# Kernel optimization log

Hardware: AMD Instinct MI355X
Metric: run time of the kernel (lower is better)

## Reference

```python
import jax, jax.numpy as jnp
import numpy as np

K = 5                      # spline kernel_size per dim
NEG = -1e30                # finite -inf stand-in for max-scatter init
_COMBO = np.indices((2, 2, 2)).reshape(3, 8).T   # [8,3] corner offsets of the deg-1 B-spline support
_STRIDE = np.array([1, K, K * K])


def spline_basis(pseudo):
    # pseudo: [E,3] in [0,1]; open degree-1 B-spline, kernel_size K per dim.
    v = jnp.clip(pseudo, 0.0, 1.0) * (K - 1)
    i0 = jnp.clip(jnp.floor(v), 0, K - 2)
    f = v - i0                                   # [E,3] fractional part
    c = jnp.asarray(_COMBO)                      # [8,3]
    w = jnp.prod(jnp.where(c[None] == 1, f[:, None, :], 1.0 - f[:, None, :]), axis=2)  # [E,8]
    k = jnp.sum((i0.astype(jnp.int32)[:, None, :] + c[None]) * jnp.asarray(_STRIDE)[None, None, :], axis=2)  # [E,8]
    return w, k


def spline_conv(x, src, dst, pseudo, W, root, bias):
    # x:[N,Fin], W:[K^3,Fin,Fout]. Gather-spline-scatter, mean aggregation + root weight + bias.
    N = x.shape[0]
    U = jnp.einsum('ni,kio->nko', x, W)          # [N,K^3,Fout] all-kernel transform (dense GEMM)
    bw, kidx = spline_basis(pseudo)              # [E,8], [E,8]
    msg = jnp.sum(bw[:, :, None] * U[src[:, None], kidx], axis=1)  # [E,Fout]
    deg = jnp.zeros((N,), x.dtype).at[dst].add(1.0)
    agg = jnp.zeros((N, W.shape[2]), x.dtype).at[dst].add(msg) / jnp.maximum(deg, 1.0)[:, None]
    return agg + x @ root + bias


def weighted_max_pool(x, w, cluster, C):
    # keep features of the max-attention-weight node in each voxel cluster
    seg_w = jnp.full((C,), NEG, x.dtype).at[cluster].max(w)
    winner = w >= seg_w[cluster]
    pooled = jnp.full((C, x.shape[1]), NEG, x.dtype).at[cluster].max(jnp.where(winner[:, None], x, NEG))
    return jnp.where(pooled <= NEG / 2, 0.0, pooled)


def dense_max_pool(x, cluster, C):
    pooled = jnp.full((C, x.shape[1]), NEG, x.dtype).at[cluster].max(x)
    return jnp.where(pooled <= NEG / 2, 0.0, pooled)


def setup_inputs() -> dict:
    key = jax.random.key(0)
    ks = iter(jax.random.split(key, 80))
    N = [30000, 10000, 4000, 1500, 600]
    E = [360000, 120000, 48000, 18000, 7200]
    Fin = [1, 32, 64, 64, 64]
    Fout = [32, 64, 64, 64, 64]
    Cs = [10000, 4000, 1500, 600, 128]
    d = {"x": jax.random.normal(next(ks), (N[0], 1), jnp.float32)}
    for l in range(5):
        d[f"src{l}"] = jax.random.randint(next(ks), (E[l],), 0, N[l], jnp.int32)
        d[f"dst{l}"] = jax.random.randint(next(ks), (E[l],), 0, N[l], jnp.int32)
        d[f"pseudo{l}"] = jax.random.uniform(next(ks), (E[l], 3), jnp.float32)
    for l in range(5):
        d[f"cluster{l+1}"] = jax.random.randint(next(ks), (N[l],), 0, Cs[l], jnp.int32)
    for l in range(5):
        d[f"W{l+1}"] = 0.1 * jax.random.normal(next(ks), (K ** 3, Fin[l], Fout[l]), jnp.float32)
        d[f"root{l+1}"] = 0.1 * jax.random.normal(next(ks), (Fin[l], Fout[l]), jnp.float32)
        d[f"b{l+1}"] = jnp.zeros((Fout[l],), jnp.float32)
    for l, fdim in enumerate([32, 64, 64, 64]):
        d[f"attw{l+1}"] = 0.1 * jax.random.normal(next(ks), (fdim, 2), jnp.float32)
        d[f"attb{l+1}"] = jnp.zeros((2,), jnp.float32)
    d["fcw"] = 0.05 * jax.random.normal(next(ks), (512, 10), jnp.float32)
    d["fcb"] = jnp.zeros((10,), jnp.float32)
    return d


def reference(x, src0, dst0, pseudo0, src1, dst1, pseudo1, src2, dst2, pseudo2,
              src3, dst3, pseudo3, src4, dst4, pseudo4,
              cluster1, cluster2, cluster3, cluster4, cluster5,
              W1, root1, b1, W2, root2, b2, W3, root3, b3, W4, root4, b4, W5, root5, b5,
              attw1, attb1, attw2, attb2, attw3, attb3, attw4, attb4, fcw, fcb):
    h = jax.nn.elu(spline_conv(x, src0, dst0, pseudo0, W1, root1, b1))
    h = weighted_max_pool(h, (h @ attw1 + attb1)[:, 0], cluster1, 10000)
    h = jax.nn.elu(spline_conv(h, src1, dst1, pseudo1, W2, root2, b2))
    h = weighted_max_pool(h, (h @ attw2 + attb2)[:, 0], cluster2, 4000)
    h = jax.nn.elu(spline_conv(h, src2, dst2, pseudo2, W3, root3, b3))
    h = weighted_max_pool(h, (h @ attw3 + attb3)[:, 0], cluster3, 1500)
    h = jax.nn.elu(spline_conv(h, src3, dst3, pseudo3, W4, root4, b4))
    h = weighted_max_pool(h, (h @ attw4 + attb4)[:, 0], cluster4, 600)
    h = jax.nn.relu(spline_conv(h, src4, dst4, pseudo4, W5, root5, b5))
    h = dense_max_pool(h, cluster5, 128)        # [128, 64] = 16 graphs x 8 voxels
    z = h.reshape(-1, 512)                      # [16, 8*64]
    return jax.nn.log_softmax(z @ fcw + fcb, axis=1)
```

## Files before the change

### kernel.cpp

```cpp
#include <hip/hip_runtime.h>
#include <math.h>

#define KS 5

typedef __bf16 bf16x8 __attribute__((ext_vector_type(8)));
typedef float f32x4 __attribute__((ext_vector_type(4)));
typedef unsigned long long u64;

__device__ __forceinline__ unsigned int flipf(float f) {
    unsigned int b = __float_as_uint(f);
    return b ^ ((b >> 31) ? 0xFFFFFFFFu : 0x80000000u);
}
__device__ __forceinline__ float unflipf(unsigned int u) {
    unsigned int b = u ^ ((u >> 31) ? 0x80000000u : 0xFFFFFFFFu);
    return __uint_as_float(b);
}
__device__ __forceinline__ float pread(unsigned int u) {
    return (u == 0u) ? 0.f : unflipf(u);
}

__device__ __forceinline__ void basis1(float p, int& b, float& f) {
    float v = fminf(fmaxf(p, 0.f), 1.f) * (float)(KS - 1);
    float fl = fminf(floorf(v), (float)(KS - 2));
    b = (int)fl; f = v - fl;
}

__device__ const int cE[5]     = {360000, 120000, 48000, 18000, 7200};
__device__ const int cN[5]     = {30000, 10000, 4000, 1500, 600};
__device__ const int cNB[5]    = {512, 469, 188, 71, 29};
__device__ const int cStart[5] = {0, 512, 981, 1169, 1240};
__device__ const int cBTend[5] = {8192, 139264, 401408, 663552, 925696};
__device__ const int cLFIN[5]  = {0, 5, 6, 6, 6};
__device__ const int cLFOUT[5] = {5, 6, 6, 6, 6};
__device__ const int sStart[4] = {0, 469, 657, 728};

#define PREP_BLOCKS  1269
#define BPACK_TOT    925696
#define BPACK_BLOCKS 3616
#define SCAT_BLOCKS  757
#define CONV0_BLOCKS 2048
#define E0           360000


struct BatchPtrs {
    const float* ps[5];
    const int*   dst[5];
    int*   cell[5];
    int*   ctrl[5];
    int*   blkbase[5];
    float* deg[5];
    float* rankf[5];
    int*   dstbase[5];
    int*   eord[5];
};

struct BpackPtrs {
    const float* W[5];
    __bf16* H[5];
    __bf16* M[5];
    __bf16* L[5];
};

__global__ void prep_bpack(BatchPtrs P, BpackPtrs B)
{
    __shared__ int lh[64];
    int blk = blockIdx.x;
    int t = threadIdx.x;

    if (blk < PREP_BLOCKS) {
        int l = (blk >= 512) + (blk >= 981) + (blk >= 1169) + (blk >= 1240);
        int lb = blk - cStart[l];
        int E = cE[l];
        int stride = cNB[l] * 256;
        const int* dst = P.dst[l];
        float* deg = P.deg[l];
        float* rankf = P.rankf[l];

        if (l == 0) {
            for (int e = lb * 256 + t; e < E; e += stride)
                rankf[e] = atomicAdd(&deg[dst[e]], 1.0f);
            return;
        }
        const float* pseudo = P.ps[l];
        int* cell = P.cell[l];
        if (t < 64) lh[t] = 0;
        __syncthreads();
        for (int e = lb * 256 + t; e < E; e += stride) {
            int b0, b1, b2; float f0, f1, f2;
            basis1(pseudo[e * 3 + 0], b0, f0);
            basis1(pseudo[e * 3 + 1], b1, f1);
            basis1(pseudo[e * 3 + 2], b2, f2);
            int c = b0 + 4 * b1 + 16 * b2;
            cell[e] = c;
            atomicAdd(&lh[c], 1);
            rankf[e] = atomicAdd(&deg[dst[e]], 1.0f);
        }
        __syncthreads();
        if (t < 64) P.blkbase[l][lb * 64 + t] = atomicAdd(&P.ctrl[l][t], lh[t]);
        return;
    }

    int tt = (blk - PREP_BLOCKS) * 256 + t;
    if (tt >= BPACK_TOT) return;
    int l = (tt >= 8192) + (tt >= 139264) + (tt >= 401408) + (tt >= 663552);
    int tl = tt - (l ? cBTend[l - 1] : 0);
    int lfout = cLFOUT[l], lfin = cLFIN[l];
    int lkb = (l == 0) ? 2 : lfin;
    int fin = 1 << lfin;
    const float* W = B.W[l];
    int o = tl & ((1 << lfout) - 1);
    int kb = (tl >> lfout) & ((1 << lkb) - 1);
    int cellid = tl >> (lfout + lkb);
    int b0 = cellid & 3, b1 = (cellid >> 2) & 3, b2 = cellid >> 4;
    bf16x8 vh, vm, vl;
    #pragma unroll
    for (int j = 0; j < 8; ++j) {
        int r = kb * 8 + j;
        float val = 0.f;
        if (r < (fin << 3)) {
            int c = r >> lfin;
            int i = r & (fin - 1);
            int k = (b0 + (c & 1)) + 5 * (b1 + ((c >> 1) & 1)) + 25 * (b2 + (c >> 2));
            val = W[((((size_t)k << lfin) + i) << lfout) + o];
        }
        __bf16 hv = (__bf16)val;
        vh[j] = hv;
        float r1 = val - (float)hv;
        __bf16 mv = (__bf16)r1;
        vm[j] = mv;
        vl[j] = (__bf16)(r1 - (float)mv);
    }
    *reinterpret_cast<bf16x8*>(B.H[l] + (size_t)tl * 8) = vh;
    *reinterpret_cast<bf16x8*>(B.M[l] + (size_t)tl * 8) = vm;
    *reinterpret_cast<bf16x8*>(B.L[l] + (size_t)tl * 8) = vl;
}

__global__ void scan5(BatchPtrs P)
{
    __shared__ int wtot[128];
    __shared__ int tots;
    int l = blockIdx.x;
    int* ctrl = P.ctrl[l];
    const float* deg = P.deg[l];
    int* dstbase = P.dstbase[l];
    int N = cN[l];

    int t = (int)threadIdx.x;
    int lane = t & 63;
    int wid = t >> 6;

    if (t < 64) {
        int h = ctrl[t];
        int x = h;
        #pragma unroll
        for (int off = 1; off < 64; off <<= 1) {
            int y = __shfl_up(x, off, 64);
            if (lane >= off) x += y;
        }
        int excl = x - h;
        ctrl[128 + t] = excl;
        int ch = (h + 63) >> 6;
        int cx = ch;
        #pragma unroll
        for (int off = 1; off < 64; off <<= 1) {
            int y = __shfl_up(cx, off, 64);
            if (lane >= off) cx += y;
        }
        ctrl[200 + t] = cx - ch;
        if (t == 63) {
            ctrl[128 + 64] = excl + h;
            ctrl[200 + 64] = cx;
            ctrl[272] = cx;
        }
    }

    int4 v0, v1, v2, v3, v4, v5, v6, v7;
    int ss[8], xs[8];
    #define LOADC(c, vr) { \
        int i0 = (c << 12) + t * 4; \
        vr = make_int4(0, 0, 0, 0); \
        if (i0 < N) { \
            float4 d = *reinterpret_cast<const float4*>(deg + i0); \
            vr.x = (int)d.x; vr.y = (int)d.y; vr.z = (int)d.z; vr.w = (int)d.w; \
        } \
        int s = vr.x + vr.y + vr.z + vr.w; \
        int x = s; \
        _Pragma("unroll") \
        for (int off = 1; off < 64; off <<= 1) { \
            int y = __shfl_up(x, off, 64); \
            if (lane >= off) x += y; \
        } \
        ss[c] = s; xs[c] = x; \
        if (lane == 63) wtot[c * 16 + wid] = x; \
    }
    LOADC(0, v0) LOADC(1, v1) LOADC(2, v2) LOADC(3, v3)
    LOADC(4, v4) LOADC(5, v5) LOADC(6, v6) LOADC(7, v7)
    #undef LOADC
    __syncthreads();
    if (t < 64) {
        int a0 = wtot[2 * t], a1 = wtot[2 * t + 1];
        int p = a0 + a1;
        int pi = p;
        #pragma unroll
        for (int off = 1; off < 64; off <<= 1) {
            int y = __shfl_up(pi, off, 64);
            if (lane >= off) pi += y;
        }
        int excl = pi - p;
        wtot[2 * t] = excl;
        wtot[2 * t + 1] = excl + a0;
        if (t == 63) tots = pi;
    }
    __syncthreads();
    #define STOREC(c, vr) { \
        int i0 = (c << 12) + t * 4; \
        if (i0 < N) { \
            int e0 = wtot[c * 16 + wid] + (xs[c] - ss[c]); \
            int4 o; \
            o.x = e0; \
            o.y = e0 + vr.x; \
            o.z = o.y + vr.y; \
            o.w = o.z + vr.z; \
            *reinterpret_cast<int4*>(dstbase + i0) = o; \
        } \
    }
    STOREC(0, v0) STOREC(1, v1) STOREC(2, v2) STOREC(3, v3)
    STOREC(4, v4) STOREC(5, v5) STOREC(6, v6) STOREC(7, v7)
    #undef STOREC
    if (t == 0) dstbase[N] = tots;
}

__global__ void scatter_conv0(BatchPtrs P,
                              const float* __restrict__ x0,
                              const int* __restrict__ src0,
                              const float* __restrict__ ps0,
                              const float* __restrict__ W0,
                              float* __restrict__ msg)
{
    __shared__ int cur[64];
    __shared__ float Wsh[4000];
    int blk = blockIdx.x;
    int t = threadIdx.x;

    if (blk < SCAT_BLOCKS) {
        int li = (blk >= 469) + (blk >= 657) + (blk >= 728);
        int l = 1 + li;
        int lb = blk - sStart[li];
        int E = cE[l];
        int stride = cNB[l] * 256;
        const int* cell = P.cell[l];
        const int* dst = P.dst[l];
        const int* dstbase = P.dstbase[l];
        float* rankf = P.rankf[l];
        int* posb = (int*)rankf;
        int* eord = P.eord[l];

        if (t < 64) cur[t] = P.ctrl[l][128 + t] + P.blkbase[l][lb * 64 + t];
        __syncthreads();
        for (int e = lb * 256 + t; e < E; e += stride) {
            int p = atomicAdd(&cur[cell[e]], 1);
            eord[p] = e;
            int r = (int)rankf[e];
            posb[e] = dstbase[dst[e]] + r;
        }
        return;
    }

    for (int i = t; i < 4000; i += 256) Wsh[i] = W0[i];
    __syncthreads();
    const int* dst0 = P.dst[0];
    const float* rank0 = P.rankf[0];
    const int* dstb0 = P.dstbase[0];
    int gs = CONV0_BLOCKS * 256;
    for (int g = (blk - SCAT_BLOCKS) * 256 + t; g < E0 * 32; g += gs) {
        int e = g >> 5;
        int o = g & 31;
        int b0, b1, b2; float f0, f1, f2;
        basis1(ps0[e * 3 + 0], b0, f0);
        basis1(ps0[e * 3 + 1], b1, f1);
        basis1(ps0[e * 3 + 2], b2, f2);
        float g0 = 1.f - f0, g1 = 1.f - f1, g2 = 1.f - f2;
        float acc = 0.f;
        #pragma unroll
        for (int c = 0; c < 8; ++c) {
            float bwc = ((c & 1) ? f0 : g0) * (((c >> 1) & 1) ? f1 : g1) * (((c >> 2) & 1) ? f2 : g2);
            int k = (b0 + (c & 1)) + 5 * (b1 + ((c >> 1) & 1)) + 25 * (b2 + (c >> 2));
            acc = fmaf(bwc, Wsh[k * 32 + o], acc);
        }
        int pos = dstb0[dst0[e]] + (int)rank0[e];
        msg[(size_t)pos * 32 + o] = x0[src0[e]] * acc;
    }
}

template<int FIN, int FOUT, bool GATHER>
__global__ void conv_mfma(const float* __restrict__ xin,
                          const u64* __restrict__ win,
                          const int* __restrict__ src,
                          const float* __restrict__ pseudo,
                          const __bf16* __restrict__ BpH,
                          const __bf16* __restrict__ BpM,
                          const __bf16* __restrict__ BpL,
                          const int* __restrict__ ctrl,
                          const int* __restrict__ eord,
                          const int* __restrict__ posb,
                          float* __restrict__ msg)
{
    constexpr int KB = FIN;
    constexpr int KSTEPS = FIN / 4;
    constexpr int NF = FOUT / 16;
    constexpr int SLICE = 4 * FOUT * 8;

    __shared__ float cst[64][FOUT + 1];
    __shared__ int posv[64];
    __shared__ __bf16 bsh[3][SLICE];

    int bid = blockIdx.x;
    if (bid >= ctrl[272]) return;
    int blo = 0, bhi = 64;
    while (blo + 1 < bhi) {
        int mid = (blo + bhi) >> 1;
        if (ctrl[200 + mid] <= bid) blo = mid; else bhi = mid;
    }
    int bucket = blo;
    int m0 = (bid - ctrl[200 + bucket]) << 6;
    int bbase = ctrl[128 + bucket];
    int bsize = ctrl[128 + bucket + 1] - bbase;

    int tt = threadIdx.x;
    int lane = tt & 63;
    int wave = tt >> 6;
    int h4 = lane >> 4;
    int col = lane & 15;
    int row = m0 + wave * 16 + col;
    bool valid = row < bsize;
    int e = eord[bbase + (valid ? row : 0)];
    int s = src[e];

    if (tt < 64) {
        int orow = m0 + tt;
        posv[tt] = (orow < bsize) ? posb[eord[bbase + orow]] : -1;
    }

    float bw[8];
    {
        int b0, b1, b2; float f0, f1, f2;
        basis1(pseudo[e * 3 + 0], b0, f0);
        basis1(pseudo[e * 3 + 1], b1, f1);
        basis1(pseudo[e * 3 + 2], b2, f2);
        float g0 = 1.f - f0, g1 = 1.f - f1, g2 = 1.f - f2;
        float vf = valid ? 1.f : 0.f;
        #pragma unroll
        for (int j = 0; j < 8; ++j)
            bw[j] = vf * ((j & 1) ? f0 : g0) * (((j >> 1) & 1) ? f1 : g1) * (((j >> 2) & 1) ? f2 : g2);
    }

    const float* xrow;
    bool xok = true;
    if (GATHER) {
        u64 wv = win[s];
        xok = (wv != 0ull);
        xrow = xin + (size_t)(unsigned int)(wv & 0xffffffffu) * FIN;
    } else {
        xrow = xin + (size_t)s * FIN;
    }

    float xv[8], xw[8];
    #pragma unroll
    for (int j = 0; j < 8; ++j) { xv[j] = 0.f; xw[j] = 0.f; }
    if (xok) {
        const float4* xb = reinterpret_cast<const float4*>(xrow + h4 * 8);
        float4 u0 = xb[0], u1 = xb[1];
        xv[0] = u0.x; xv[1] = u0.y; xv[2] = u0.z; xv[3] = u0.w;
        xv[4] = u1.x; xv[5] = u1.y; xv[6] = u1.z; xv[7] = u1.w;
        if (FIN == 64) {
            const float4* xb2 = reinterpret_cast<const float4*>(xrow + 32 + h4 * 8);
            float4 w0 = xb2[0], w1 = xb2[1];
            xw[0] = w0.x; xw[1] = w0.y; xw[2] = w0.z; xw[3] = w0.w;
            xw[4] = w1.x; xw[5] = w1.y; xw[6] = w1.z; xw[7] = w1.w;
        }
    }

    f32x4 acc[NF];
    #pragma unroll
    for (int nf = 0; nf < NF; ++nf) acc[nf] = (f32x4){0.f, 0.f, 0.f, 0.f};

    for (int kt = 0; kt < KSTEPS; ++kt) {
        __syncthreads();
        {
            size_t gbase = ((size_t)bucket * KB + kt * 4) * FOUT * 8;
            int idx = tt * 8;
            if (idx < SLICE) {
                *reinterpret_cast<bf16x8*>(&bsh[0][idx]) =
                    *reinterpret_cast<const bf16x8*>(BpH + gbase + idx);
                *reinterpret_cast<bf16x8*>(&bsh[1][idx]) =
                    *reinterpret_cast<const bf16x8*>(BpM + gbase + idx);
                *reinterpret_cast<bf16x8*>(&bsh[2][idx]) =
                    *reinterpret_cast<const bf16x8*>(BpL + gbase + idx);
            }
        }
        __syncthreads();

        float v[8];
        if (FIN == 64) {
            float bwc = bw[kt >> 1];
            const float* u = (kt & 1) ? xw : xv;
            #pragma unroll
            for (int j = 0; j < 8; ++j) v[j] = u[j] * bwc;
        } else {
            float bwc = bw[kt];
            #pragma unroll
            for (int j = 0; j < 8; ++j) v[j] = xv[j] * bwc;
        }
        bf16x8 ah, am, al;
        #pragma unroll
        for (int j = 0; j < 8; ++j) {
            __bf16 hv = (__bf16)v[j];
            ah[j] = hv;
            float r1 = v[j] - (float)hv;
            __bf16 mv = (__bf16)r1;
            am[j] = mv;
            al[j] = (__bf16)(r1 - (float)mv);
        }
        #pragma unroll
        for (int nf = 0; nf < NF; ++nf) {
            int loff = (h4 * FOUT + nf * 16 + col) * 8;
            bf16x8 bh = *reinterpret_cast<const bf16x8*>(&bsh[0][loff]);
            bf16x8 bm = *reinterpret_cast<const bf16x8*>(&bsh[1][loff]);
            bf16x8 bl = *reinterpret_cast<const bf16x8*>(&bsh[2][loff]);
            acc[nf] = __builtin_amdgcn_mfma_f32_16x16x32_bf16(ah, bh, acc[nf], 0, 0, 0);
            acc[nf] = __builtin_amdgcn_mfma_f32_16x16x32_bf16(ah, bm, acc[nf], 0, 0, 0);
            acc[nf] = __builtin_amdgcn_mfma_f32_16x16x32_bf16(am, bh, acc[nf], 0, 0, 0);
            acc[nf] = __builtin_amdgcn_mfma_f32_16x16x32_bf16(am, bm, acc[nf], 0, 0, 0);
            acc[nf] = __builtin_amdgcn_mfma_f32_16x16x32_bf16(ah, bl, acc[nf], 0, 0, 0);
            acc[nf] = __builtin_amdgcn_mfma_f32_16x16x32_bf16(al, bh, acc[nf], 0, 0, 0);
        }
    }

    #pragma unroll
    for (int nf = 0; nf < NF; ++nf)
        #pragma unroll
        for (int j = 0; j < 4; ++j)
            cst[wave * 16 + h4 * 4 + j][nf * 16 + col] = acc[nf][j];
    __syncthreads();

    constexpr int F4 = FOUT / 4;
    constexpr int ITER = 64 * F4 / 256;
    #pragma unroll
    for (int i = 0; i < ITER; ++i) {
        int idx = i * 256 + tt;
        int r = idx / F4;
        int c4 = idx - r * F4;
        int p = posv[r];
        if (p >= 0) {
            float4 vq = make_float4(cst[r][c4 * 4], cst[r][c4 * 4 + 1],
                                    cst[r][c4 * 4 + 2], cst[r][c4 * 4 + 3]);
            *reinterpret_cast<float4*>(msg + (size_t)p * FOUT + c4 * 4) = vq;
        }
    }
}

template<int FIN, int FOUT, int ACT, int POOLMODE, bool GATHER>
__global__ void node_finalize(const float* __restrict__ xin,
                              const u64* __restrict__ winprev,
                              const float* __restrict__ msg,
                              const int* __restrict__ dstbase,
                              const float* __restrict__ deg,
                              const float* __restrict__ root,
                              const float* __restrict__ bias,
                              const float* __restrict__ attw,
                              const float* __restrict__ attb,
                              const int* __restrict__ cluster,
                              float* __restrict__ out,
                              u64* __restrict__ seg64,
                              unsigned int* __restrict__ pooled,
                              int N)
{
    int t = blockIdx.x * blockDim.x + threadIdx.x;
    int n = t / FOUT, o = t % FOUT;
    if (n >= N) return;
    int b0 = dstbase[n];
    int dn = (int)deg[n];
    float a = 0.f;
    for (int r = 0; r < dn; ++r)
        a += msg[(size_t)(b0 + r) * FOUT + o];
    a = a / fmaxf((float)dn, 1.f) + bias[o];

    const float* xrow;
    bool xok = true;
    if (GATHER) {
        u64 wv = winprev[n];
        xok = (wv != 0ull);
        xrow = xin + (size_t)(unsigned int)(wv & 0xffffffffu) * FIN;
    } else {
        xrow = xin + (size_t)n * FIN;
    }
    if (xok) {
        #pragma unroll
        for (int i = 0; i < FIN; ++i)
            a = fmaf(xrow[i], root[i * FOUT + o], a);
    }
    if (ACT == 0) a = (a > 0.f) ? a : expm1f(a);
    else          a = fmaxf(a, 0.f);
    if (POOLMODE == 1) {
        atomicMax(&pooled[(size_t)cluster[n] * FOUT + o], flipf(a));
        return;
    }
    out[t] = a;
    float w = a * attw[2 * o];
    #pragma unroll
    for (int off = FOUT / 2; off >= 1; off >>= 1)
        w += __shfl_xor(w, off, 64);
    if (o == 0) {
        float wt = w + attb[0];
        u64 key = ((u64)flipf(wt) << 32) | (unsigned int)n;
        atomicMax(&seg64[cluster[n]], key);
    }
}

__global__ void pool_final_fc(const unsigned int* __restrict__ pooled,
                              const float* __restrict__ fcw,
                              const float* __restrict__ fcb,
                              float* __restrict__ out)
{
    __shared__ float h[8192];
    __shared__ float logits[16][10];
    __shared__ float lse[16];
    int t = threadIdx.x;
    for (int i = t; i < 8192; i += 512)
        h[i] = pread(pooled[i]);
    __syncthreads();
    if (t < 160) {
        int g = t / 10, cls = t - g * 10;
        float a = fcb[cls];
        for (int j = 0; j < 512; ++j)
            a = fmaf(h[g * 512 + j], fcw[j * 10 + cls], a);
        logits[g][cls] = a;
    }
    __syncthreads();
    if (t < 16) {
        float m = -1e30f;
        for (int c = 0; c < 10; ++c) m = fmaxf(m, logits[t][c]);
        float s = 0.f;
        for (int c = 0; c < 10; ++c) s += expf(logits[t][c] - m);
        lse[t] = m + logf(s);
    }
    __syncthreads();
    if (t < 160) out[t] = logits[t / 10][t - (t / 10) * 10] - lse[t / 10];
}

static const int hE[5] = {360000, 120000, 48000, 18000, 7200};
static const int hN[5] = {30000, 10000, 4000, 1500, 600};

#define OFF_HA     0
#define OFF_HB     960000
#define OFF_DEG    1600000
#define OFF_CTRL   1646112
#define OFF_SEG64  1648672
#define OFF_POOL4  1680880
#define ZERO_FLTS  89072
#define OFF_BLK    1689072
#define OFF_DSTB   1770288
#define OFF_CELL   1816464
#define OFF_RANK   2369680
#define OFF_EORD   2922896
#define OFF_BP     3476112
#define OFF_MSG    14584464

static const int cumN_h[5]    = {0, 30000, 40000, 44000, 45500};
static const int cumC_h[5]    = {0, 10000, 14000, 15500, 16100};
static const int cumBLK_h[5]  = {0, 32768, 62784, 74816, 79360};
static const int cumDSTB_h[5] = {0, 30016, 40032, 44048, 45568};
static const int cumE_h[5]    = {0, 360000, 480000, 528000, 546000};
static const size_t planeB_h[5] = {65536, 1048576, 2097152, 2097152, 2097152};
static const size_t cumBPf_h[5] = {0, 98304, 1671168, 4816896, 7962624};

extern "C" void kernel_launch(void* const* d_in, const int* in_sizes, int n_in,
                              void* d_out, int out_size, void* d_ws, size_t ws_size,
                              hipStream_t stream)
{
    const float* x0 = (const float*)d_in[0];
    const int*   src_[5]  = {(const int*)d_in[1], (const int*)d_in[4], (const int*)d_in[7], (const int*)d_in[10], (const int*)d_in[13]};
    const int*   dst_[5]  = {(const int*)d_in[2], (const int*)d_in[5], (const int*)d_in[8], (const int*)d_in[11], (const int*)d_in[14]};
    const float* ps_[5]   = {(const float*)d_in[3], (const float*)d_in[6], (const float*)d_in[9], (const float*)d_in[12], (const float*)d_in[15]};
    const int*   cl_[5]   = {(const int*)d_in[16], (const int*)d_in[17], (const int*)d_in[18], (const int*)d_in[19], (const int*)d_in[20]};
    const float* W_[5]    = {(const float*)d_in[21], (const float*)d_in[24], (const float*)d_in[27], (const float*)d_in[30], (const float*)d_in[33]};
    const float* root_[5] = {(const float*)d_in[22], (const float*)d_in[25], (const float*)d_in[28], (const float*)d_in[31], (const float*)d_in[34]};
    const float* b_[5]    = {(const float*)d_in[23], (const float*)d_in[26], (const float*)d_in[29], (const float*)d_in[32], (const float*)d_in[35]};
    const float* attw_[4] = {(const float*)d_in[36], (const float*)d_in[38], (const float*)d_in[40], (const float*)d_in[42]};
    const float* attb_[4] = {(const float*)d_in[37], (const float*)d_in[39], (const float*)d_in[41], (const float*)d_in[43]};
    const float* fcw = (const float*)d_in[44];
    const float* fcb = (const float*)d_in[45];

    float* ws_f = (float*)d_ws;
    float* hA = ws_f + OFF_HA;
    float* hB = ws_f + OFF_HB;
    float* msg = ws_f + OFF_MSG;
    unsigned int* pool4 = (unsigned int*)(ws_f + OFF_POOL4);

    BatchPtrs P;
    BpackPtrs BP;
    const __bf16* BpH_l[5]; const __bf16* BpM_l[5]; const __bf16* BpL_l[5];
    int* ctrl_l[5]; int* dstb_l[5]; int* eord_l[5]; int* posb_l[5];
    float* deg_l[5];
    u64* seg64_l[5];
    for (int l = 0; l < 5; ++l) {
        P.ps[l] = ps_[l];
        P.dst[l] = dst_[l];
        P.cell[l] = (int*)(ws_f + OFF_CELL + cumE_h[l]);
        P.ctrl[l] = (int*)(ws_f + OFF_CTRL + l * 512);
        P.blkbase[l] = (int*)(ws_f + OFF_BLK + cumBLK_h[l]);
        P.deg[l] = ws_f + OFF_DEG + cumN_h[l];
        P.rankf[l] = ws_f + OFF_RANK + cumE_h[l];
        P.dstbase[l] = (int*)(ws_f + OFF_DSTB + cumDSTB_h[l]);
        P.eord[l] = (int*)(ws_f + OFF_EORD + cumE_h[l]);
        __bf16* H = (__bf16*)(ws_f + OFF_BP + cumBPf_h[l]);
        BP.W[l] = W_[l];
        BP.H[l] = H;
        BP.M[l] = H + planeB_h[l];
        BP.L[l] = H + 2 * planeB_h[l];
        BpH_l[l] = BP.H[l]; BpM_l[l] = BP.M[l]; BpL_l[l] = BP.L[l];
        ctrl_l[l] = P.ctrl[l];
        dstb_l[l] = P.dstbase[l];
        eord_l[l] = P.eord[l];
        posb_l[l] = (int*)P.rankf[l];
        deg_l[l] = P.deg[l];
        seg64_l[l] = (u64*)(ws_f + OFF_SEG64) + cumC_h[l];
    }

    (void)hipMemsetAsync(ws_f + OFF_DEG, 0, (size_t)ZERO_FLTS * 4, stream);
    prep_bpack<<<PREP_BLOCKS + BPACK_BLOCKS, 256, 0, stream>>>(P, BP);
    scan5<<<5, 1024, 0, stream>>>(P);
    scatter_conv0<<<SCAT_BLOCKS + CONV0_BLOCKS, 256, 0, stream>>>(
        P, x0, src_[0], ps_[0], W_[0], msg);

    node_finalize<1, 32, 0, 0, false><<<(hN[0] * 32) / 256, 256, 0, stream>>>(
        x0, nullptr, msg, dstb_l[0], deg_l[0], root_[0], b_[0], attw_[0], attb_[0], cl_[0], hA, seg64_l[0], nullptr, hN[0]);

    conv_mfma<32, 64, true><<<hE[1] / 64 + 65, 256, 0, stream>>>(
        hA, seg64_l[0], src_[1], ps_[1], BpH_l[1], BpM_l[1], BpL_l[1], ctrl_l[1], eord_l[1], posb_l[1], msg);
    node_finalize<32, 64, 0, 0, true><<<(hN[1] * 64) / 256, 256, 0, stream>>>(
        hA, seg64_l[0], msg, dstb_l[1], deg_l[1], root_[1], b_[1], attw_[1], attb_[1], cl_[1], hB, seg64_l[1], nullptr, hN[1]);

    conv_mfma<64, 64, true><<<hE[2] / 64 + 65, 256, 0, stream>>>(
        hB, seg64_l[1], src_[2], ps_[2], BpH_l[2], BpM_l[2], BpL_l[2], ctrl_l[2], eord_l[2], posb_l[2], msg);
    node_finalize<64, 64, 0, 0, true><<<(hN[2] * 64) / 256, 256, 0, stream>>>(
        hB, seg64_l[1], msg, dstb_l[2], deg_l[2], root_[2], b_[2], attw_[2], attb_[2], cl_[2], hA, seg64_l[2], nullptr, hN[2]);

    conv_mfma<64, 64, true><<<hE[3] / 64 + 65, 256, 0, stream>>>(
        hA, seg64_l[2], src_[3], ps_[3], BpH_l[3], BpM_l[3], BpL_l[3], ctrl_l[3], eord_l[3], posb_l[3], msg);
    node_finalize<64, 64, 0, 0, true><<<(hN[3] * 64) / 256, 256, 0, stream>>>(
        hA, seg64_l[2], msg, dstb_l[3], deg_l[3], root_[3], b_[3], attw_[3], attb_[3], cl_[3], hB, seg64_l[3], nullptr, hN[3]);

    conv_mfma<64, 64, true><<<hE[4] / 64 + 65, 256, 0, stream>>>(
        hB, seg64_l[3], src_[4], ps_[4], BpH_l[4], BpM_l[4], BpL_l[4], ctrl_l[4], eord_l[4], posb_l[4], msg);
    node_finalize<64, 64, 1, 1, true><<<(hN[4] * 64) / 256, 256, 0, stream>>>(
        hB, seg64_l[3], msg, dstb_l[4], deg_l[4], root_[4], b_[4], nullptr, nullptr, cl_[4], nullptr, nullptr, pool4, hN[4]);
    pool_final_fc<<<1, 512, 0, stream>>>(pool4, fcw, fcb, (float*)d_out);
}
```

Before: 277.0 us.

## Pack spline weights per kernel index instead of per cell, shrinking prep

The weight prepack previously expanded W into 64 cell-specific copies (each cell holding the 8 corner kernels), writing about 925k bf16x8 vectors across three split planes. It now packs each of the 125 kernel slices once, transposed to [k][o][i], and the conv kernel computes the corner kernel index from the bucket id to fetch the right slice. This cuts prep work and workspace traffic substantially and improves cache reuse of packed weights. Layer 0 packing is dropped, which assumes the conv0 path does not use these buffers.

Measured after the change: 279.8 us. About the same (+1.0%).

```diff
diff --git a/kernel.cpp b/kernel.cpp
--- a/kernel.cpp
+++ b/kernel.cpp
@@ -29,14 +29,11 @@
 __device__ const int cN[5]     = {30000, 10000, 4000, 1500, 600};
 __device__ const int cNB[5]    = {512, 469, 188, 71, 29};
 __device__ const int cStart[5] = {0, 512, 981, 1169, 1240};
-__device__ const int cBTend[5] = {8192, 139264, 401408, 663552, 925696};
-__device__ const int cLFIN[5]  = {0, 5, 6, 6, 6};
-__device__ const int cLFOUT[5] = {5, 6, 6, 6, 6};
 __device__ const int sStart[4] = {0, 469, 657, 728};
 
 #define PREP_BLOCKS  1269
-#define BPACK_TOT    925696
-#define BPACK_BLOCKS 3616
+#define BPACK_TOT    224000
+#define BPACK_BLOCKS 875
 #define SCAT_BLOCKS  757
 #define CONV0_BLOCKS 2048
 #define E0           360000
@@ -100,29 +97,22 @@
         return;
     }
 
-    int tt = (blk - PREP_BLOCKS) * 256 + t;
-    if (tt >= BPACK_TOT) return;
-    int l = (tt >= 8192) + (tt >= 139264) + (tt >= 401408) + (tt >= 663552);
-    int tl = tt - (l ? cBTend[l - 1] : 0);
-    int lfout = cLFOUT[l], lfin = cLFIN[l];
-    int lkb = (l == 0) ? 2 : lfin;
-    int fin = 1 << lfin;
+    int u = (blk - PREP_BLOCKS) * 256 + t;
+    if (u >= BPACK_TOT) return;
+    int l = 1 + (u >= 32000) + (u >= 96000) + (u >= 160000);
+    int ul = u - ((l == 1) ? 0 : (l == 2) ? 32000 : (l == 3) ? 96000 : 160000);
+    int fin = (l == 1) ? 32 : 64;
+    int i8 = fin >> 3;
+    int iu = ul % i8;
+    int rest = ul / i8;
+    int o = rest & 63;
+    int k = rest >> 6;
     const float* W = B.W[l];
-    int o = tl & ((1 << lfout) - 1);
-    int kb = (tl >> lfout) & ((1 << lkb) - 1);
-    int cellid = tl >> (lfout + lkb);
-    int b0 = cellid & 3, b1 = (cellid >> 2) & 3, b2 = cellid >> 4;
+    int i0 = iu * 8;
     bf16x8 vh, vm, vl;
     #pragma unroll
     for (int j = 0; j < 8; ++j) {
-        int r = kb * 8 + j;
-        float val = 0.f;
-        if (r < (fin << 3)) {
-            int c = r >> lfin;
-            int i = r & (fin - 1);
-            int k = (b0 + (c & 1)) + 5 * (b1 + ((c >> 1) & 1)) + 25 * (b2 + (c >> 2));
-            val = W[((((size_t)k << lfin) + i) << lfout) + o];
-        }
+        float val = W[((size_t)k * fin + i0 + j) * 64 + o];
         __bf16 hv = (__bf16)val;
         vh[j] = hv;
         float r1 = val - (float)hv;
@@ -130,9 +120,10 @@
         vm[j] = mv;
         vl[j] = (__bf16)(r1 - (float)mv);
     }
-    *reinterpret_cast<bf16x8*>(B.H[l] + (size_t)tl * 8) = vh;
-    *reinterpret_cast<bf16x8*>(B.M[l] + (size_t)tl * 8) = vm;
-    *reinterpret_cast<bf16x8*>(B.L[l] + (size_t)tl * 8) = vl;
+    size_t doff = ((size_t)k * 64 + o) * fin + i0;
+    *reinterpret_cast<bf16x8*>(B.H[l] + doff) = vh;
+    *reinterpret_cast<bf16x8*>(B.M[l] + doff) = vm;
+    *reinterpret_cast<bf16x8*>(B.L[l] + doff) = vl;
 }
 
 __global__ void scan5(BatchPtrs P)
@@ -305,7 +296,6 @@
                           const int* __restrict__ posb,
                           float* __restrict__ msg)
 {
-    constexpr int KB = FIN;
     constexpr int KSTEPS = FIN / 4;
     constexpr int NF = FOUT / 16;
     constexpr int SLICE = 4 * FOUT * 8;
@@ -325,6 +315,7 @@
     int m0 = (bid - ctrl[200 + bucket]) << 6;
     int bbase = ctrl[128 + bucket];
     int bsize = ctrl[128 + bucket + 1] - bbase;
+    int cb0 = bucket & 3, cb1 = (bucket >> 2) & 3, cb2 = bucket >> 4;
 
     int tt = threadIdx.x;
     int lane = tt & 63;
@@ -384,18 +375,25 @@
     #pragma unroll
     for (int nf = 0; nf < NF; ++nf) acc[nf] = (f32x4){0.f, 0.f, 0.f, 0.f};
 
+    int h4u = tt / FOUT;
+    int ou = tt % FOUT;
+
     for (int kt = 0; kt < KSTEPS; ++kt) {
+        int c = (FIN == 64) ? (kt >> 1) : kt;
+        int k = (cb0 + (c & 1)) + 5 * (cb1 + ((c >> 1) & 1)) + 25 * (cb2 + (c >> 2));
+        int ibase = (FIN == 64) ? ((kt & 1) * 32) : 0;
+        size_t g = ((size_t)k * FOUT + ou) * FIN + ibase + h4u * 8;
+
         __syncthreads();
         {
-            size_t gbase = ((size_t)bucket * KB + kt * 4) * FOUT * 8;
             int idx = tt * 8;
             if (idx < SLICE) {
                 *reinterpret_cast<bf16x8*>(&bsh[0][idx]) =
-                    *reinterpret_cast<const bf16x8*>(BpH + gbase + idx);
+                    *reinterpret_cast<const bf16x8*>(BpH + g);
                 *reinterpret_cast<bf16x8*>(&bsh[1][idx]) =
-                    *reinterpret_cast<const bf16x8*>(BpM + gbase + idx);
+                    *reinterpret_cast<const bf16x8*>(BpM + g);
                 *reinterpret_cast<bf16x8*>(&bsh[2][idx]) =
-                    *reinterpret_cast<const bf16x8*>(BpL + gbase + idx);
+                    *reinterpret_cast<const bf16x8*>(BpL + g);
             }
         }
         __syncthreads();
@@ -571,8 +569,8 @@
 static const int cumBLK_h[5]  = {0, 32768, 62784, 74816, 79360};
 static const int cumDSTB_h[5] = {0, 30016, 40032, 44048, 45568};
 static const int cumE_h[5]    = {0, 360000, 480000, 528000, 546000};
-static const size_t planeB_h[5] = {65536, 1048576, 2097152, 2097152, 2097152};
-static const size_t cumBPf_h[5] = {0, 98304, 1671168, 4816896, 7962624};
+static const size_t planeB_h[5] = {0, 256000, 512000, 512000, 512000};
+static const size_t cumBPf_h[5] = {0, 0, 384000, 1152000, 1920000};
 
 extern "C" void kernel_launch(void* const* d_in, const int* in_sizes, int n_in,
                               void* d_out, int out_size, void* d_ws, size_t ws_size,
```
